# Kernel tuning notes

Measured on AMD Instinct MI355X. Metric: run time of the kernel, lower is better.

## Reference

```python
import jax, jax.numpy as jnp
import numpy as np

N = 100000   # nodes
E = 1600000  # edges
F = 128      # input features
D = 128      # hidden dim
L = 3        # layers
G = 128      # graphs in batch
C = 2        # classes
BN_EPS = 1e-5


def setup_inputs() -> dict:
    key = jax.random.key(0)
    ks = jax.random.split(key, 20)
    s = 1.0 / np.sqrt(D)
    inp = {
        "x": jax.random.normal(ks[0], (N, F), jnp.float32),
        "edge_index": jax.random.randint(ks[1], (2, E), 0, N),
        "node_weight": jax.random.uniform(ks[2], (N,), jnp.float32),
        "batch": jnp.sort(jax.random.randint(ks[3], (N,), 0, G)),
        # GIN MLP params, stacked over layers (all square since F == D)
        "W1": jax.random.normal(ks[4], (L, F, D), jnp.float32) * s,
        "b1": jnp.zeros((L, D), jnp.float32),
        "g1": jnp.ones((L, D), jnp.float32),
        "bt1": jnp.zeros((L, D), jnp.float32),
        "W2": jax.random.normal(ks[5], (L, D, D), jnp.float32) * s,
        "b2": jnp.zeros((L, D), jnp.float32),
        "g2": jnp.ones((L, D), jnp.float32),
        "bt2": jnp.zeros((L, D), jnp.float32),
        # outer per-layer BatchNorm
        "og": jnp.ones((L, D), jnp.float32),
        "ob": jnp.zeros((L, D), jnp.float32),
        # final classifier
        "fcW": jax.random.normal(ks[6], (D, C), jnp.float32) * s,
        "fcb": jnp.zeros((C,), jnp.float32),
    }
    return inp


def _bn(h, gamma, beta):
    # training-mode BatchNorm1d over nodes: biased variance, eps=1e-5
    m = jnp.mean(h, axis=0)
    v = jnp.var(h, axis=0)
    return (h - m) * jax.lax.rsqrt(v + BN_EPS) * gamma + beta


def reference(x, edge_index, node_weight, batch,
              W1, b1, g1, bt1, W2, b2, g2, bt2, og, ob, fcW, fcb):
    src, dst = edge_index[0], edge_index[1]  # messages flow src -> dst (PyG)
    for l in range(L):
        # GIN: sum_{j in N(i)} x_j + (1 + eps) * x_i,  eps = 0 (non-trainable)
        agg = jax.ops.segment_sum(x[src], dst, num_segments=N)
        h = agg + x
        # nn = Linear -> BN -> Linear -> BN
        h = _bn(h @ W1[l] + b1[l], g1[l], bt1[l])
        h = _bn(h @ W2[l] + b2[l], g2[l], bt2[l])
        # outer BN + ReLU (dropout p=0 is identity)
        x = jax.nn.relu(_bn(h, og[l], ob[l]))
    node_embeddings = x
    graph_embedding = jax.ops.segment_sum(
        node_embeddings * node_weight[:, None], batch, num_segments=G)
    out = graph_embedding @ fcW + fcb
    return (node_embeddings, graph_embedding, out)
```

## Files before the change

kernel.cpp:

```cpp
#include <hip/hip_runtime.h>

#define N_NODES 100000
#define N_EDGES 1600000
#define DF 128
#define NL 3
#define NG 128
#define NC 2
#define BN_EPS 1e-5f
#define GEMM_BLOCKS ((N_NODES + 127) / 128)
#define GE_SLICES 16

#define NBKT 98
#define NBIN_BLOCKS 512
#define EDGES_PER_BLOCK (N_EDGES / NBIN_BLOCKS)

typedef unsigned int u32;
typedef unsigned short u16;
typedef unsigned long long u64;

using bf16x8 = __attribute__((ext_vector_type(8))) short;
using f32x4  = __attribute__((ext_vector_type(4))) float;

__device__ __forceinline__ u16 f2bf(float f) {
    u32 u = __float_as_uint(f);
    u32 r = (u + 0x7FFFu + ((u >> 16) & 1u)) >> 16;
    return (u16)r;
}
__device__ __forceinline__ float bflo(u32 v) { return __uint_as_float(v << 16); }
__device__ __forceinline__ float bfhi(u32 v) { return __uint_as_float(v & 0xFFFF0000u); }

__global__ __launch_bounds__(256) void cvt_x_kernel(const float* __restrict__ x,
                                                    u16* __restrict__ xb) {
    size_t i4 = (size_t)blockIdx.x * 256 + threadIdx.x;
    float4 v = ((const float4*)x)[i4];
    u32 lo = (u32)f2bf(v.x) | ((u32)f2bf(v.y) << 16);
    u32 hi = (u32)f2bf(v.z) | ((u32)f2bf(v.w) << 16);
    ((uint2*)xb)[i4] = make_uint2(lo, hi);
}

__global__ __launch_bounds__(256) void bin_count_kernel(const int* __restrict__ dst,
                                                        int* __restrict__ blkhist) {
    __shared__ int hist[NBKT];
    int t = threadIdx.x, b = blockIdx.x;
    for (int i = t; i < NBKT; i += 256) hist[i] = 0;
    __syncthreads();
    int base = b * EDGES_PER_BLOCK;
    for (int i = t; i < EDGES_PER_BLOCK; i += 256)
        atomicAdd(&hist[dst[base + i] >> 10], 1);
    __syncthreads();
    for (int i = t; i < NBKT; i += 256) blkhist[i * NBIN_BLOCKS + b] = hist[i];
}

__global__ __launch_bounds__(512) void binscanA_kernel(int* __restrict__ blkhist,
                                                       int* __restrict__ bkt_total) {
    __shared__ int buf[NBIN_BLOCKS];
    int bucket = blockIdx.x, t = threadIdx.x;
    int v = blkhist[bucket * NBIN_BLOCKS + t];
    buf[t] = v;
    __syncthreads();
    for (int off = 1; off < NBIN_BLOCKS; off <<= 1) {
        int tv = (t >= off) ? buf[t - off] : 0;
        __syncthreads();
        buf[t] += tv;
        __syncthreads();
    }
    blkhist[bucket * NBIN_BLOCKS + t] = buf[t] - v;
    if (t == NBIN_BLOCKS - 1) bkt_total[bucket] = buf[t];
}

__global__ __launch_bounds__(128) void binscanB_kernel(const int* __restrict__ bkt_total,
                                                       int* __restrict__ bktbase) {
    __shared__ int buf[128];
    int t = threadIdx.x;
    int v = (t < NBKT) ? bkt_total[t] : 0;
    buf[t] = v;
    __syncthreads();
    for (int off = 1; off < 128; off <<= 1) {
        int tv = (t >= off) ? buf[t - off] : 0;
        __syncthreads();
        buf[t] += tv;
        __syncthreads();
    }
    if (t < NBKT) bktbase[t] = buf[t] - v;
    if (t == NBKT - 1) bktbase[NBKT] = buf[t];
}

__global__ __launch_bounds__(256) void bin_scatter_kernel(const int* __restrict__ src,
                                                          const int* __restrict__ dst,
                                                          const int* __restrict__ blkhist,
                                                          const int* __restrict__ bktbase,
                                                          u64* __restrict__ pairs) {
    __shared__ int lofs[NBKT];
    int t = threadIdx.x, b = blockIdx.x;
    for (int i = t; i < NBKT; i += 256)
        lofs[i] = bktbase[i] + blkhist[i * NBIN_BLOCKS + b];
    __syncthreads();
    int base = b * EDGES_PER_BLOCK;
    for (int i = t; i < EDGES_PER_BLOCK; i += 256) {
        int d = dst[base + i];
        int s = src[base + i];
        int p = atomicAdd(&lofs[d >> 10], 1);
        pairs[p] = ((u64)(u32)d << 32) | (u32)s;
    }
}

__global__ __launch_bounds__(1024) void csr_build_kernel(const u64* __restrict__ pairs,
                                                         const int* __restrict__ bktbase,
                                                         int* __restrict__ offsets,
                                                         int* __restrict__ adj) {
    __shared__ int cnt[1024];
    __shared__ int buf[1024];
    int b = blockIdx.x, t = threadIdx.x;
    int nbase = b << 10;
    int pb = bktbase[b], pe = bktbase[b + 1];
    cnt[t] = 0;
    __syncthreads();
    for (int i = pb + t; i < pe; i += 1024)
        atomicAdd(&cnt[(int)(pairs[i] >> 32) - nbase], 1);
    __syncthreads();
    int v = cnt[t];
    buf[t] = v;
    __syncthreads();
    for (int off = 1; off < 1024; off <<= 1) {
        int tv = (t >= off) ? buf[t - off] : 0;
        __syncthreads();
        buf[t] += tv;
        __syncthreads();
    }
    int excl = buf[t] - v;
    int node = nbase + t;
    if (node < N_NODES) offsets[node] = pb + excl;
    if (b == NBKT - 1 && t == 0) offsets[N_NODES] = N_EDGES;
    cnt[t] = excl;
    __syncthreads();
    for (int i = pb + t; i < pe; i += 1024) {
        u64 pr = pairs[i];
        int d = (int)(pr >> 32);
        int pos = atomicAdd(&cnt[d - nbase], 1);
        adj[pb + pos] = (int)(pr & 0xFFFFFFFFu);
    }
}

__global__ __launch_bounds__(256) void agg_kernel(const u32* __restrict__ X,
                                                  const int* __restrict__ offsets,
                                                  const int* __restrict__ adj,
                                                  u32* __restrict__ out) {
    int node = blockIdx.x * 4 + (threadIdx.x >> 6);
    int l = threadIdx.x & 63;
    const u32* Xl = X + l;
    u32 v = Xl[(size_t)node << 6];
    float s0 = bflo(v), s1 = bfhi(v);
    float t0 = 0.f, t1 = 0.f;
    int k = offsets[node], e = offsets[node + 1];
    for (; k + 16 <= e; k += 16) {
        int a[16];
#pragma unroll
        for (int i = 0; i < 16; i++) a[i] = adj[k + i];
        u32 u[16];
#pragma unroll
        for (int i = 0; i < 16; i++) u[i] = Xl[(size_t)a[i] << 6];
#pragma unroll
        for (int i = 0; i < 16; i += 2) {
            s0 += bflo(u[i]);     s1 += bfhi(u[i]);
            t0 += bflo(u[i + 1]); t1 += bfhi(u[i + 1]);
        }
    }
    if (k + 8 <= e) {
        int a[8];
#pragma unroll
        for (int i = 0; i < 8; i++) a[i] = adj[k + i];
        u32 u[8];
#pragma unroll
        for (int i = 0; i < 8; i++) u[i] = Xl[(size_t)a[i] << 6];
#pragma unroll
        for (int i = 0; i < 8; i += 2) {
            s0 += bflo(u[i]);     s1 += bfhi(u[i]);
            t0 += bflo(u[i + 1]); t1 += bfhi(u[i + 1]);
        }
        k += 8;
    }
    if (k + 4 <= e) {
        int a0 = adj[k + 0], a1 = adj[k + 1], a2 = adj[k + 2], a3 = adj[k + 3];
        u32 u0 = Xl[(size_t)a0 << 6];
        u32 u1 = Xl[(size_t)a1 << 6];
        u32 u2 = Xl[(size_t)a2 << 6];
        u32 u3 = Xl[(size_t)a3 << 6];
        s0 += bflo(u0); s1 += bfhi(u0);
        t0 += bflo(u1); t1 += bfhi(u1);
        s0 += bflo(u2); s1 += bfhi(u2);
        t0 += bflo(u3); t1 += bfhi(u3);
        k += 4;
    }
    for (; k < e; k++) {
        u32 u = Xl[(size_t)adj[k] << 6];
        s0 += bflo(u); s1 += bfhi(u);
    }
    out[((size_t)node << 6) + l] = (u32)f2bf(s0 + t0) | ((u32)f2bf(s1 + t1) << 16);
}

template <int OUT_BF16>
__global__ __launch_bounds__(256) void gemm_mfma_kernel(const u16* __restrict__ A,
                                                        const u16* __restrict__ Wt,
                                                        const float* __restrict__ bias,
                                                        void* __restrict__ outp,
                                                        float* __restrict__ psumB,
                                                        float* __restrict__ psqB, int nrows) {
    __shared__ __align__(16) u16 sW[16384];

    int tid = threadIdx.x;
    int rb = blockIdx.x * 128;

    {
        const uint4* g = (const uint4*)Wt;
#pragma unroll
        for (int p = 0; p < 8; p++) {
            int q = p * 256 + tid;
            int r = q >> 4, seg = q & 15;
            uint4 v = g[q];
            *(uint4*)((char*)sW + r * 256 + ((seg * 16) ^ ((r & 7) << 4))) = v;
        }
    }

    int l = tid & 63, w = tid >> 6;
    int lr = l & 15, lg = l >> 4;

    bf16x8 afr[2][4];
#pragma unroll
    for (int t = 0; t < 2; t++) {
        int grow = rb + w * 32 + t * 16 + lr;
        bool ok = grow < nrows;
#pragma unroll
        for (int kc = 0; kc < 4; kc++) {
            bf16x8 z = {0, 0, 0, 0, 0, 0, 0, 0};
            if (ok) z = *(const bf16x8*)(A + (size_t)grow * 128 + kc * 32 + lg * 8);
            afr[t][kc] = z;
        }
    }
    __syncthreads();

    f32x4 acc[2][8];
#pragma unroll
    for (int t = 0; t < 2; t++)
#pragma unroll
        for (int c = 0; c < 8; c++) acc[t][c] = (f32x4){0.f, 0.f, 0.f, 0.f};

#pragma unroll
    for (int kc = 0; kc < 4; kc++) {
        int kb2 = (kc * 32 + lg * 8) * 2;
        bf16x8 b[8];
#pragma unroll
        for (int c = 0; c < 8; c++) {
            int col = c * 16 + lr;
            b[c] = *(const bf16x8*)((const char*)sW + col * 256 + (kb2 ^ ((col & 7) << 4)));
        }
#pragma unroll
        for (int t = 0; t < 2; t++)
#pragma unroll
            for (int c = 0; c < 8; c++)
                acc[t][c] = __builtin_amdgcn_mfma_f32_16x16x32_bf16(afr[t][kc], b[c], acc[t][c], 0, 0, 0);
    }

    float bb[8];
#pragma unroll
    for (int c = 0; c < 8; c++) bb[c] = bias[c * 16 + lr];

    float sp[8], qp[8];
#pragma unroll
    for (int c = 0; c < 8; c++) { sp[c] = 0.f; qp[c] = 0.f; }

    float* outF = (float*)outp;
    u16* outB = (u16*)outp;
#pragma unroll
    for (int t = 0; t < 2; t++) {
#pragma unroll
        for (int r = 0; r < 4; r++) {
            int grow = rb + w * 32 + t * 16 + lg * 4 + r;
            bool ok = grow < nrows;
#pragma unroll
            for (int c = 0; c < 8; c++) {
                float v = acc[t][c][r] + bb[c];
                if (ok) {
                    int col = c * 16 + lr;
                    if (OUT_BF16)
                        outB[(size_t)grow * 128 + col] = f2bf(v);
                    else
                        outF[(size_t)grow * 128 + col] = v;
                    sp[c] += v;
                    qp[c] += v * v;
                }
            }
        }
    }
#pragma unroll
    for (int c = 0; c < 8; c++) {
        sp[c] += __shfl_xor(sp[c], 16); sp[c] += __shfl_xor(sp[c], 32);
        qp[c] += __shfl_xor(qp[c], 16); qp[c] += __shfl_xor(qp[c], 32);
    }
    __syncthreads();
    float* sred = (float*)sW;
    if (lg == 0) {
#pragma unroll
        for (int c = 0; c < 8; c++) {
            sred[(((w * 8 + c) * 16) + lr) * 2 + 0] = sp[c];
            sred[(((w * 8 + c) * 16) + lr) * 2 + 1] = qp[c];
        }
    }
    __syncthreads();
    if (tid < 128) {
        int c = tid >> 4, r = tid & 15;
        float s = 0.f, q = 0.f;
#pragma unroll
        for (int ww = 0; ww < 4; ww++) {
            s += sred[(((ww * 8 + c) * 16) + r) * 2 + 0];
            q += sred[(((ww * 8 + c) * 16) + r) * 2 + 1];
        }
        psumB[blockIdx.x * 128 + tid] = s;
        psqB[blockIdx.x * 128 + tid] = q;
    }
}

template <int MODE>
__global__ __launch_bounds__(256) void stats_reduce_kernel(const float* __restrict__ psumB,
                                                           const float* __restrict__ psqB,
                                                           const float* __restrict__ g,
                                                           const float* __restrict__ bt,
                                                           const float* __restrict__ og,
                                                           const float* __restrict__ ob,
                                                           float* __restrict__ outS,
                                                           float* __restrict__ outQ) {
    int f = blockIdx.x;
    int t = threadIdx.x;
    float s = 0.f, q = 0.f;
    for (int b = t; b < GEMM_BLOCKS; b += 256) {
        s += psumB[b * 128 + f];
        q += psqB[b * 128 + f];
    }
#pragma unroll
    for (int off = 1; off < 64; off <<= 1) {
        s += __shfl_xor(s, off);
        q += __shfl_xor(q, off);
    }
    __shared__ float rs[4], rq[4];
    int w = t >> 6;
    if ((t & 63) == 0) { rs[w] = s; rq[w] = q; }
    __syncthreads();
    if (t == 0) {
        float S = rs[0] + rs[1] + rs[2] + rs[3];
        float Q = rq[0] + rq[1] + rq[2] + rq[3];
        if (MODE == 0) {
            outS[f] = S;
            outQ[f] = Q;
        } else {
            float m = S / (float)N_NODES;
            float v = Q / (float)N_NODES - m * m;
            if (v < 0.f) v = 0.f;
            float r2 = rsqrtf(v + BN_EPS);
            float a = r2 * g[f];
            float vu = v * a * a;
            float r3 = rsqrtf(vu + BN_EPS);
            float sc = a * r3 * og[f];
            outS[f] = sc;
            outQ[f] = ob[f] - m * sc;
        }
    }
}

__global__ __launch_bounds__(128) void bnfold_kernel(const float* __restrict__ psum,
                                                     const float* __restrict__ psq,
                                                     const float* __restrict__ g,
                                                     const float* __restrict__ bt,
                                                     const float* __restrict__ W2,
                                                     const float* __restrict__ b2,
                                                     u16* __restrict__ W2ft,
                                                     float* __restrict__ b2f) {
    __shared__ float sc1[128], sh1[128];
    int k = threadIdx.x;
    int j = blockIdx.x;
    {
        float S = psum[k], Q = psq[k];
        float m = S / (float)N_NODES;
        float v = Q / (float)N_NODES - m * m;
        if (v < 0.f) v = 0.f;
        float r = rsqrtf(v + BN_EPS);
        float sc = r * g[k];
        sc1[k] = sc;
        sh1[k] = bt[k] - m * sc;
    }
    __syncthreads();
    float w = W2[k * 128 + j];
    W2ft[j * 128 + k] = f2bf(sc1[k] * w);
    float p = sh1[k] * w;
#pragma unroll
    for (int off = 1; off < 64; off <<= 1) p += __shfl_xor(p, off);
    __shared__ float r2[2];
    if ((k & 63) == 0) r2[k >> 6] = p;
    __syncthreads();
    if (k == 0) b2f[j] = b2[j] + r2[0] + r2[1];
}

__global__ void w1_prep_kernel(const float* __restrict__ W, u16* __restrict__ Wt) {
    int q = blockIdx.x * 256 + threadIdx.x;
    int layer = q >> 14;
    int r = q & 16383;
    int j = r >> 7, k = r & 127;
    Wt[q] = f2bf(W[layer * 16384 + k * 128 + j]);
}

__global__ __launch_bounds__(256) void relu_affine_bf16_kernel(const u16* __restrict__ Hb,
                                                               const float* __restrict__ scale,
                                                               const float* __restrict__ shift,
                                                               u16* __restrict__ xb) {
    size_t i4 = (size_t)blockIdx.x * 256 + threadIdx.x;
    int fb = ((int)(i4 & 31)) * 4;
    uint2 hv = ((const uint2*)Hb)[i4];
    float4 sc = *(const float4*)&scale[fb];
    float4 sh = *(const float4*)&shift[fb];
    float y0 = fmaxf(bflo(hv.x) * sc.x + sh.x, 0.f);
    float y1 = fmaxf(bfhi(hv.x) * sc.y + sh.y, 0.f);
    float y2 = fmaxf(bflo(hv.y) * sc.z + sh.z, 0.f);
    float y3 = fmaxf(bfhi(hv.y) * sc.w + sh.w, 0.f);
    u32 lo = (u32)f2bf(y0) | ((u32)f2bf(y1) << 16);
    u32 hi = (u32)f2bf(y2) | ((u32)f2bf(y3) << 16);
    ((uint2*)xb)[i4] = make_uint2(lo, hi);
}

__global__ __launch_bounds__(256) void relu_affine_final_kernel(float* __restrict__ H,
                                                                const float* __restrict__ scale,
                                                                const float* __restrict__ shift) {
    size_t i4 = (size_t)blockIdx.x * 256 + threadIdx.x;
    int fb = ((int)(i4 & 31)) * 4;
    float4 h = ((const float4*)H)[i4];
    float4 sc = *(const float4*)&scale[fb];
    float4 sh = *(const float4*)&shift[fb];
    float4 y;
    y.x = fmaxf(h.x * sc.x + sh.x, 0.f);
    y.y = fmaxf(h.y * sc.y + sh.y, 0.f);
    y.z = fmaxf(h.z * sc.z + sh.z, 0.f);
    y.w = fmaxf(h.w * sc.w + sh.w, 0.f);
    ((float4*)H)[i4] = y;
}

__global__ __launch_bounds__(128) void graph_embed_part_kernel(const float* __restrict__ X,
                                                               const float* __restrict__ w,
                                                               const int* __restrict__ batch,
                                                               float* __restrict__ gpart) {
    int g = blockIdx.x;
    int sl = blockIdx.y;
    int f = threadIdx.x;
    int lo = 0, hi = N_NODES;
    while (lo < hi) { int mid = (lo + hi) >> 1; if (batch[mid] < g) lo = mid + 1; else hi = mid; }
    int s = lo;
    lo = 0; hi = N_NODES;
    while (lo < hi) { int mid = (lo + hi) >> 1; if (batch[mid] < g + 1) lo = mid + 1; else hi = mid; }
    int e = lo;
    int cnt = e - s;
    int per = (cnt + GE_SLICES - 1) / GE_SLICES;
    int rs = s + sl * per;
    int re = rs + per; if (re > e) re = e;
    float acc = 0.f;
    for (int r = rs; r < re; r++) acc += X[(size_t)r * DF + f] * w[r];
    gpart[((size_t)g * GE_SLICES + sl) * DF + f] = acc;
}

__global__ __launch_bounds__(128) void graph_embed_reduce_kernel(const float* __restrict__ gpart,
                                                                 float* __restrict__ ge) {
    int g = blockIdx.x, f = threadIdx.x;
    float a = 0.f;
#pragma unroll
    for (int s = 0; s < GE_SLICES; s++) a += gpart[((size_t)g * GE_SLICES + s) * DF + f];
    ge[g * DF + f] = a;
}

__global__ void final_fc_kernel(const float* __restrict__ ge, const float* __restrict__ fcW,
                                const float* __restrict__ fcb, float* __restrict__ out) {
    int idx = blockIdx.x * blockDim.x + threadIdx.x;
    if (idx < NG * NC) {
        int g = idx / NC, c = idx % NC;
        float acc = fcb[c];
        for (int d = 0; d < DF; d++) acc += ge[g * DF + d] * fcW[d * NC + c];
        out[idx] = acc;
    }
}

extern "C" void kernel_launch(void* const* d_in, const int* in_sizes, int n_in,
                              void* d_out, int out_size, void* d_ws, size_t ws_size,
                              hipStream_t stream) {
    const float* x    = (const float*)d_in[0];
    const int*   ei   = (const int*)d_in[1];
    const int*   src  = ei;
    const int*   dst  = ei + N_EDGES;
    const float* nw   = (const float*)d_in[2];
    const int*   batch= (const int*)d_in[3];
    const float* W1   = (const float*)d_in[4];
    const float* b1   = (const float*)d_in[5];
    const float* g1   = (const float*)d_in[6];
    const float* bt1  = (const float*)d_in[7];
    const float* W2   = (const float*)d_in[8];
    const float* b2   = (const float*)d_in[9];
    const float* g2   = (const float*)d_in[10];
    const float* bt2  = (const float*)d_in[11];
    const float* og   = (const float*)d_in[12];
    const float* ob   = (const float*)d_in[13];
    const float* fcW  = (const float*)d_in[14];
    const float* fcb  = (const float*)d_in[15];

    float* out_f    = (float*)d_out;
    float* node_out = out_f;
    float* ge       = out_f + (size_t)N_NODES * DF;
    float* cls      = ge + NG * DF;

    char* w = (char*)d_ws;
    auto alloc = [&](size_t bytes) { char* p = w; w += (bytes + 255) & ~(size_t)255; return p; };

    u16*   XB      = (u16*)alloc((size_t)N_NODES * DF * 2);
    u16*   AGG     = (u16*)alloc((size_t)N_NODES * DF * 2);
    u16*   H1      = (u16*)alloc((size_t)N_NODES * DF * 2);
    int*   offsets = (int*)alloc((size_t)(N_NODES + 1) * 4);
    int*   adj     = (int*)alloc((size_t)N_EDGES * 4);
    float* psumB   = (float*)alloc((size_t)GEMM_BLOCKS * 128 * 4);
    float* psqB    = (float*)alloc((size_t)GEMM_BLOCKS * 128 * 4);
    float* sF      = (float*)alloc(128 * 4);
    float* qF      = (float*)alloc(128 * 4);
    u16*   W1t     = (u16*)alloc((size_t)NL * 16384 * 2);
    u16*   W2ft    = (u16*)alloc(16384 * 2);
    float* b2f     = (float*)alloc(128 * 4);
    float* scaleO  = (float*)alloc(128 * 4);
    float* shiftO  = (float*)alloc(128 * 4);
    float* gpart   = (float*)alloc((size_t)NG * GE_SLICES * DF * 4);
    int*   blkhist = (int*)alloc((size_t)NBKT * NBIN_BLOCKS * 4);
    int*   bkt_tot = (int*)alloc(NBKT * 4);
    int*   bktbase = (int*)alloc((NBKT + 1) * 4);

    u64* pairs = (u64*)AGG;

    cvt_x_kernel<<<12500, 256, 0, stream>>>(x, XB);
    w1_prep_kernel<<<192, 256, 0, stream>>>(W1, W1t);

    bin_count_kernel<<<NBIN_BLOCKS, 256, 0, stream>>>(dst, blkhist);
    binscanA_kernel<<<NBKT, NBIN_BLOCKS, 0, stream>>>(blkhist, bkt_tot);
    binscanB_kernel<<<1, 128, 0, stream>>>(bkt_tot, bktbase);
    bin_scatter_kernel<<<NBIN_BLOCKS, 256, 0, stream>>>(src, dst, blkhist, bktbase, pairs);
    csr_build_kernel<<<NBKT, 1024, 0, stream>>>(pairs, bktbase, offsets, adj);

    for (int l = 0; l < NL; l++) {
        agg_kernel<<<N_NODES / 4, 256, 0, stream>>>((const u32*)XB, offsets, adj, (u32*)AGG);
        gemm_mfma_kernel<1><<<GEMM_BLOCKS, 256, 0, stream>>>(AGG, W1t + (size_t)l * 16384,
                                                             b1 + l * DF, H1, psumB, psqB,
                                                             N_NODES);
        stats_reduce_kernel<0><<<128, 256, 0, stream>>>(psumB, psqB, nullptr, nullptr,
                                                        nullptr, nullptr, sF, qF);
        bnfold_kernel<<<128, 128, 0, stream>>>(sF, qF, g1 + l * DF, bt1 + l * DF,
                                               W2 + (size_t)l * DF * DF, b2 + l * DF, W2ft, b2f);
        if (l < NL - 1) {
            gemm_mfma_kernel<1><<<GEMM_BLOCKS, 256, 0, stream>>>(H1, W2ft, b2f, AGG,
                                                                 psumB, psqB, N_NODES);
        } else {
            gemm_mfma_kernel<0><<<GEMM_BLOCKS, 256, 0, stream>>>(H1, W2ft, b2f, node_out,
                                                                 psumB, psqB, N_NODES);
        }
        stats_reduce_kernel<1><<<128, 256, 0, stream>>>(psumB, psqB, g2 + l * DF, bt2 + l * DF,
                                                        og + l * DF, ob + l * DF, scaleO, shiftO);
        if (l < NL - 1) {
            relu_affine_bf16_kernel<<<12500, 256, 0, stream>>>(AGG, scaleO, shiftO, XB);
        } else {
            relu_affine_final_kernel<<<12500, 256, 0, stream>>>(node_out, scaleO, shiftO);
        }
    }

    graph_embed_part_kernel<<<dim3(NG, GE_SLICES), 128, 0, stream>>>(node_out, nw, batch, gpart);
    graph_embed_reduce_kernel<<<NG, 128, 0, stream>>>(gpart, ge);
    final_fc_kernel<<<1, 256, 0, stream>>>(ge, fcW, fcb, cls);
}
```

Baseline: 461.0 us.

## Stage bf16 GEMM output through LDS, fuse stats reduce into bnfold, shrink agg unroll

The bf16 GEMM epilogue now writes results into swizzled shared memory and then stores full 16-byte rows coalesced to global memory, replacing scattered 2-byte stores. The first per-layer stats reduction kernel is removed: bnfold now reduces the per-block partial sums itself, with each of its 128 blocks serially looping over all 782 GEMM blocks. The aggregation loop's unroll drops from 16 to 8 edges. The redundant serial reduction in bnfold could add latency, and the extra LDS buffer raises shared memory use per GEMM block.

```diff
diff --git a/kernel.cpp b/kernel.cpp
--- a/kernel.cpp
+++ b/kernel.cpp
@@ -152,20 +152,7 @@
     float s0 = bflo(v), s1 = bfhi(v);
     float t0 = 0.f, t1 = 0.f;
     int k = offsets[node], e = offsets[node + 1];
-    for (; k + 16 <= e; k += 16) {
-        int a[16];
-#pragma unroll
-        for (int i = 0; i < 16; i++) a[i] = adj[k + i];
-        u32 u[16];
-#pragma unroll
-        for (int i = 0; i < 16; i++) u[i] = Xl[(size_t)a[i] << 6];
-#pragma unroll
-        for (int i = 0; i < 16; i += 2) {
-            s0 += bflo(u[i]);     s1 += bfhi(u[i]);
-            t0 += bflo(u[i + 1]); t1 += bfhi(u[i + 1]);
-        }
-    }
-    if (k + 8 <= e) {
+    for (; k + 8 <= e; k += 8) {
         int a[8];
 #pragma unroll
         for (int i = 0; i < 8; i++) a[i] = adj[k + i];
@@ -177,7 +164,6 @@
             s0 += bflo(u[i]);     s1 += bfhi(u[i]);
             t0 += bflo(u[i + 1]); t1 += bfhi(u[i + 1]);
         }
-        k += 8;
     }
     if (k + 4 <= e) {
         int a0 = adj[k + 0], a1 = adj[k + 1], a2 = adj[k + 2], a3 = adj[k + 3];
@@ -206,6 +192,7 @@
                                                         float* __restrict__ psumB,
                                                         float* __restrict__ psqB, int nrows) {
     __shared__ __align__(16) u16 sW[16384];
+    __shared__ float sred[1024];
 
     int tid = threadIdx.x;
     int rb = blockIdx.x * 128;
@@ -268,36 +255,62 @@
 #pragma unroll
     for (int c = 0; c < 8; c++) { sp[c] = 0.f; qp[c] = 0.f; }
 
-    float* outF = (float*)outp;
-    u16* outB = (u16*)outp;
-#pragma unroll
-    for (int t = 0; t < 2; t++) {
-#pragma unroll
-        for (int r = 0; r < 4; r++) {
-            int grow = rb + w * 32 + t * 16 + lg * 4 + r;
-            bool ok = grow < nrows;
-#pragma unroll
-            for (int c = 0; c < 8; c++) {
-                float v = acc[t][c][r] + bb[c];
-                if (ok) {
+    if (OUT_BF16) {
+        __syncthreads();
+#pragma unroll
+        for (int t = 0; t < 2; t++) {
+#pragma unroll
+            for (int r = 0; r < 4; r++) {
+                int row = w * 32 + t * 16 + lg * 4 + r;
+                bool ok = (rb + row) < nrows;
+#pragma unroll
+                for (int c = 0; c < 8; c++) {
+                    float v = acc[t][c][r] + bb[c];
                     int col = c * 16 + lr;
-                    if (OUT_BF16)
-                        outB[(size_t)grow * 128 + col] = f2bf(v);
-                    else
-                        outF[(size_t)grow * 128 + col] = v;
-                    sp[c] += v;
-                    qp[c] += v * v;
+                    *(u16*)((char*)sW + ((row * 256 + col * 2) ^ ((row & 7) << 4))) = f2bf(v);
+                    if (ok) { sp[c] += v; qp[c] += v * v; }
                 }
             }
         }
-    }
+        __syncthreads();
+        u16* outB = (u16*)outp;
+#pragma unroll
+        for (int p = 0; p < 8; p++) {
+            int q = p * 256 + tid;
+            int row = q >> 4, seg = q & 15;
+            int grow = rb + row;
+            if (grow < nrows) {
+                uint4 v = *(const uint4*)((char*)sW + ((row * 256 + seg * 16) ^ ((row & 7) << 4)));
+                *(uint4*)(outB + (size_t)grow * 128 + seg * 8) = v;
+            }
+        }
+    } else {
+        float* outF = (float*)outp;
+#pragma unroll
+        for (int t = 0; t < 2; t++) {
+#pragma unroll
+            for (int r = 0; r < 4; r++) {
+                int grow = rb + w * 32 + t * 16 + lg * 4 + r;
+                bool ok = grow < nrows;
+#pragma unroll
+                for (int c = 0; c < 8; c++) {
+                    float v = acc[t][c][r] + bb[c];
+                    if (ok) {
+                        outF[(size_t)grow * 128 + c * 16 + lr] = v;
+                        sp[c] += v;
+                        qp[c] += v * v;
+                    }
+                }
+            }
+        }
+    }
+
 #pragma unroll
     for (int c = 0; c < 8; c++) {
         sp[c] += __shfl_xor(sp[c], 16); sp[c] += __shfl_xor(sp[c], 32);
         qp[c] += __shfl_xor(qp[c], 16); qp[c] += __shfl_xor(qp[c], 32);
     }
-    __syncthreads();
-    float* sred = (float*)sW;
+    if (OUT_BF16) __syncthreads();
     if (lg == 0) {
 #pragma unroll
         for (int c = 0; c < 8; c++) {
@@ -319,15 +332,14 @@
     }
 }
 
-template <int MODE>
-__global__ __launch_bounds__(256) void stats_reduce_kernel(const float* __restrict__ psumB,
-                                                           const float* __restrict__ psqB,
-                                                           const float* __restrict__ g,
-                                                           const float* __restrict__ bt,
-                                                           const float* __restrict__ og,
-                                                           const float* __restrict__ ob,
-                                                           float* __restrict__ outS,
-                                                           float* __restrict__ outQ) {
+__global__ __launch_bounds__(256) void stats_reduce_fin2_kernel(const float* __restrict__ psumB,
+                                                                const float* __restrict__ psqB,
+                                                                const float* __restrict__ g,
+                                                                const float* __restrict__ bt,
+                                                                const float* __restrict__ og,
+                                                                const float* __restrict__ ob,
+                                                                float* __restrict__ scale,
+                                                                float* __restrict__ shift) {
     int f = blockIdx.x;
     int t = threadIdx.x;
     float s = 0.f, q = 0.f;
@@ -347,26 +359,21 @@
     if (t == 0) {
         float S = rs[0] + rs[1] + rs[2] + rs[3];
         float Q = rq[0] + rq[1] + rq[2] + rq[3];
-        if (MODE == 0) {
-            outS[f] = S;
-            outQ[f] = Q;
-        } else {
-            float m = S / (float)N_NODES;
-            float v = Q / (float)N_NODES - m * m;
-            if (v < 0.f) v = 0.f;
-            float r2 = rsqrtf(v + BN_EPS);
-            float a = r2 * g[f];
-            float vu = v * a * a;
-            float r3 = rsqrtf(vu + BN_EPS);
-            float sc = a * r3 * og[f];
-            outS[f] = sc;
-            outQ[f] = ob[f] - m * sc;
-        }
-    }
-}
-
-__global__ __launch_bounds__(128) void bnfold_kernel(const float* __restrict__ psum,
-                                                     const float* __restrict__ psq,
+        float m = S / (float)N_NODES;
+        float v = Q / (float)N_NODES - m * m;
+        if (v < 0.f) v = 0.f;
+        float r2 = rsqrtf(v + BN_EPS);
+        float a = r2 * g[f];
+        float vu = v * a * a;
+        float r3 = rsqrtf(vu + BN_EPS);
+        float sc = a * r3 * og[f];
+        scale[f] = sc;
+        shift[f] = ob[f] - m * sc;
+    }
+}
+
+__global__ __launch_bounds__(128) void bnfold_kernel(const float* __restrict__ psumB,
+                                                     const float* __restrict__ psqB,
                                                      const float* __restrict__ g,
                                                      const float* __restrict__ bt,
                                                      const float* __restrict__ W2,
@@ -377,7 +384,11 @@
     int k = threadIdx.x;
     int j = blockIdx.x;
     {
-        float S = psum[k], Q = psq[k];
+        float S = 0.f, Q = 0.f;
+        for (int b = 0; b < GEMM_BLOCKS; b++) {
+            S += psumB[b * 128 + k];
+            Q += psqB[b * 128 + k];
+        }
         float m = S / (float)N_NODES;
         float v = Q / (float)N_NODES - m * m;
         if (v < 0.f) v = 0.f;
@@ -519,8 +530,6 @@
     int*   adj     = (int*)alloc((size_t)N_EDGES * 4);
     float* psumB   = (float*)alloc((size_t)GEMM_BLOCKS * 128 * 4);
     float* psqB    = (float*)alloc((size_t)GEMM_BLOCKS * 128 * 4);
-    float* sF      = (float*)alloc(128 * 4);
-    float* qF      = (float*)alloc(128 * 4);
     u16*   W1t     = (u16*)alloc((size_t)NL * 16384 * 2);
     u16*   W2ft    = (u16*)alloc(16384 * 2);
     float* b2f     = (float*)alloc(128 * 4);
@@ -547,9 +556,7 @@
         gemm_mfma_kernel<1><<<GEMM_BLOCKS, 256, 0, stream>>>(AGG, W1t + (size_t)l * 16384,
                                                              b1 + l * DF, H1, psumB, psqB,
                                                              N_NODES);
-        stats_reduce_kernel<0><<<128, 256, 0, stream>>>(psumB, psqB, nullptr, nullptr,
-                                                        nullptr, nullptr, sF, qF);
-        bnfold_kernel<<<128, 128, 0, stream>>>(sF, qF, g1 + l * DF, bt1 + l * DF,
+        bnfold_kernel<<<128, 128, 0, stream>>>(psumB, psqB, g1 + l * DF, bt1 + l * DF,
                                                W2 + (size_t)l * DF * DF, b2 + l * DF, W2ft, b2f);
         if (l < NL - 1) {
             gemm_mfma_kernel<1><<<GEMM_BLOCKS, 256, 0, stream>>>(H1, W2ft, b2f, AGG,
@@ -558,8 +565,9 @@
             gemm_mfma_kernel<0><<<GEMM_BLOCKS, 256, 0, stream>>>(H1, W2ft, b2f, node_out,
                                                                  psumB, psqB, N_NODES);
         }
-        stats_reduce_kernel<1><<<128, 256, 0, stream>>>(psumB, psqB, g2 + l * DF, bt2 + l * DF,
-                                                        og + l * DF, ob + l * DF, scaleO, shiftO);
+        stats_reduce_fin2_kernel<<<128, 256, 0, stream>>>(psumB, psqB, g2 + l * DF, bt2 + l * DF,
+                                                          og + l * DF, ob + l * DF,
+                                                          scaleO, shiftO);
         if (l < NL - 1) {
             relu_affine_bf16_kernel<<<12500, 256, 0, stream>>>(AGG, scaleO, shiftO, XB);
         } else {
```

Measured after the change: 771.4 us. +67.3%, slower.
